# Optimization experiments

Measured on AMD Instinct MI355X. Metric: run time of the kernel, lower is better.

## Reference

```python
import jax, jax.numpy as jnp
import numpy as np

N_HEAD = 16

def setup_inputs() -> dict:
    key = jax.random.key(0)
    k1, k2, k3, k4, k5 = jax.random.split(key, 5)
    B, S, D = 2, 2048, 1024
    return {
        "hidden_states": jax.random.normal(k1, (B, S, D), jnp.float32),
        "w_attn": jax.random.normal(k2, (D, 3 * D), jnp.float32) * 0.02,
        "b_attn": jax.random.normal(k3, (3 * D,), jnp.float32) * 0.02,
        "w_proj": jax.random.normal(k4, (D, D), jnp.float32) * 0.02,
        "b_proj": jax.random.normal(k5, (D,), jnp.float32) * 0.02,
    }

def reference(hidden_states, w_attn, b_attn, w_proj, b_proj):
    B, S, D = hidden_states.shape
    H = N_HEAD
    Dh = D // H
    qkv = hidden_states @ w_attn + b_attn              # [B,S,3D]
    q, k, v = jnp.split(qkv, 3, axis=-1)
    def split_heads(x):
        return x.reshape(B, S, H, Dh).transpose(0, 2, 1, 3)  # [B,H,S,Dh]
    q, k, v = split_heads(q), split_heads(k), split_heads(v)
    # scale=True: divide by sqrt(head_dim) (v.size(-1))
    scores = jnp.einsum("bhqd,bhkd->bhqk", q, k) / jnp.sqrt(jnp.float32(Dh))
    attn = jax.nn.softmax(scores, axis=-1)             # [B,H,S,S]
    out = jnp.einsum("bhqk,bhkd->bhqd", attn, v)       # [B,H,S,Dh]
    out = out.transpose(0, 2, 1, 3).reshape(B, S, D)   # merge heads
    return out @ w_proj + b_proj
```

## Files before the change

### kernel.cpp

```cpp
#include <hip/hip_runtime.h>
#include <hip/hip_bf16.h>

typedef __attribute__((ext_vector_type(8))) short bf16x8;
typedef __attribute__((ext_vector_type(4))) float f32x4;
typedef __attribute__((ext_vector_type(16))) float f32x16;

#define LOG2E 1.4426950408889634f
#define SCALE_F (0.125f * LOG2E)

__device__ inline unsigned short f2bf(float f) {
  union { float f; unsigned u; } x; x.f = f;
  unsigned u = x.u;
  unsigned r = u + 0x7FFFu + ((u >> 16) & 1u);
  return (unsigned short)(r >> 16);
}

__device__ inline unsigned cvtpk(float lo, float hi) {
  unsigned r;
  asm("v_cvt_pk_bf16_f32 %0, %1, %2" : "=v"(r) : "v"(lo), "v"(hi));
  return r;
}

__device__ inline void gload16(const unsigned short* g, unsigned short* l) {
  __builtin_amdgcn_global_load_lds(
      (const __attribute__((address_space(1))) unsigned int*)g,
      (__attribute__((address_space(3))) unsigned int*)l, 16, 0, 0);
}

template <int J>
__device__ inline bf16x8 pack_pfrag(f32x16 p) {
  int X, Y, Z, W;
  asm("v_cvt_pk_bf16_f32 %0, %1, %2" : "=v"(X) : "v"(p[J + 0]), "v"(p[J + 1]));
  asm("v_cvt_pk_bf16_f32 %0, %1, %2" : "=v"(Y) : "v"(p[J + 2]), "v"(p[J + 3]));
  asm("v_cvt_pk_bf16_f32 %0, %1, %2" : "=v"(Z) : "v"(p[J + 4]), "v"(p[J + 5]));
  asm("v_cvt_pk_bf16_f32 %0, %1, %2" : "=v"(W) : "v"(p[J + 6]), "v"(p[J + 7]));
  asm("v_permlane32_swap_b32 %0, %1" : "+v"(X), "+v"(Z));
  asm("v_permlane32_swap_b32 %0, %1" : "+v"(Y), "+v"(W));
  union { int w[4]; bf16x8 v; } u;
  u.w[0] = X; u.w[1] = Y; u.w[2] = Z; u.w[3] = W;
  return u.v;
}

__device__ inline void transpose_tile(const float* __restrict__ W,
                                      unsigned short* __restrict__ WT, int K, int N,
                                      int n0, int k0, int t,
                                      unsigned short (*Tl)[72]) {
#pragma unroll
  for (int i = 0; i < 4; ++i) {
    int idx = t + i * 256;
    int r = idx >> 4, c4 = (idx & 15) << 2;
    float4 v = *reinterpret_cast<const float4*>(&W[(size_t)(k0 + r) * N + n0 + c4]);
    Tl[c4 + 0][r] = f2bf(v.x);
    Tl[c4 + 1][r] = f2bf(v.y);
    Tl[c4 + 2][r] = f2bf(v.z);
    Tl[c4 + 3][r] = f2bf(v.w);
  }
  __syncthreads();
#pragma unroll
  for (int i = 0; i < 2; ++i) {
    int idx = t + i * 256;
    int rr = idx >> 3, cc = (idx & 7) << 3;
    *reinterpret_cast<int4*>(&WT[(size_t)(n0 + rr) * K + k0 + cc]) =
        *reinterpret_cast<const int4*>(&Tl[rr][cc]);
  }
}

__global__ __launch_bounds__(256) void prep_fused(
    const float* __restrict__ hs, unsigned short* __restrict__ hs_b,
    const float* __restrict__ w_attn, unsigned short* __restrict__ wT,
    const float* __restrict__ w_proj, unsigned short* __restrict__ pT) {
  __shared__ unsigned short Tl[64][72];
  const int bid = blockIdx.x, t = threadIdx.x;
  if (bid < 768) {
    transpose_tile(w_attn, wT, 1024, 3072, (bid % 48) * 64, (bid / 48) * 64, t, Tl);
  } else if (bid < 1024) {
    int r = bid - 768;
    transpose_tile(w_proj, pT, 1024, 1024, (r % 16) * 64, (r / 16) * 64, t, Tl);
  } else {
    int cb = bid - 1024;
#pragma unroll
    for (int j = 0; j < 4; ++j) {
      int i = cb * 1024 + j * 256 + t;
      float4 v = reinterpret_cast<const float4*>(hs)[i];
      ushort4 o;
      o.x = f2bf(v.x); o.y = f2bf(v.y); o.z = f2bf(v.z); o.w = f2bf(v.w);
      reinterpret_cast<ushort4*>(hs_b)[i] = o;
    }
  }
}

__global__ __launch_bounds__(512, 2) void gemm_qkv_8p(
    const unsigned short* __restrict__ A, const unsigned short* __restrict__ Bt,
    const float* __restrict__ bias,
    unsigned short* __restrict__ qw, unsigned short* __restrict__ kw,
    unsigned short* __restrict__ vtg) {
  __shared__ unsigned short Abuf[2][16384];
  __shared__ unsigned short Bbuf[2][12288];
  const int t = threadIdx.x, lane = t & 63, wid = t >> 6;
  const int wm = wid >> 2, wn = wid & 3;
  const int orig = blockIdx.x;
  const int nid = (orig & 7) * 32 + (orig >> 3);
  const int mt = nid >> 4, nt = nid & 15;
  const int row0 = mt * 256, col0 = nt * 192;
  const int lr = lane & 15, kq = lane >> 4;
  const int srow_lo = lane >> 3;
  const int scg = (lane & 7) ^ srow_lo;
  const unsigned short* Ab = A + (size_t)row0 * 1024;
  const unsigned short* Bb = Bt + (size_t)col0 * 1024;
  f32x4 acc[8][3] = {};

#define SA8(bs, kt)                                                              \
  {                                                                              \
    const unsigned short* Ap = Ab + (kt) * 64;                                   \
    _Pragma("unroll") for (int i = 0; i < 4; ++i) {                              \
      int g = wid * 4 + i;                                                       \
      int rrel = g * 8 + srow_lo;                                                \
      gload16(&Ap[(size_t)rrel * 1024 + scg * 8], &Abuf[bs][g * 512]);           \
    }                                                                            \
  }
#define SB8(bs, kt)                                                              \
  {                                                                              \
    const unsigned short* Bp = Bb + (kt) * 64;                                   \
    _Pragma("unroll") for (int i = 0; i < 3; ++i) {                              \
      int g = wid * 3 + i;                                                       \
      int rrel = g * 8 + srow_lo;                                                \
      gload16(&Bp[(size_t)rrel * 1024 + scg * 8], &Bbuf[bs][g * 512]);           \
    }                                                                            \
  }
#define RDA(dst, mh)                                                             \
  _Pragma("unroll") for (int m = 0; m < 4; ++m)                                  \
  _Pragma("unroll") for (int ks = 0; ks < 2; ++ks) {                             \
    int row = wm * 128 + (mh) * 64 + m * 16 + lr;                                \
    dst[m][ks] = *reinterpret_cast<const bf16x8*>(                               \
        &Ac[row * 64 + (((ks * 4 + kq) ^ (row & 7)) << 3)]);                     \
  }
#define RDB2(dst)                                                                \
  _Pragma("unroll") for (int n = 0; n < 2; ++n)                                  \
  _Pragma("unroll") for (int ks = 0; ks < 2; ++ks) {                             \
    int row = wn * 48 + n * 16 + lr;                                             \
    dst[n][ks] = *reinterpret_cast<const bf16x8*>(                               \
        &Bc[row * 64 + (((ks * 4 + kq) ^ (row & 7)) << 3)]);                     \
  }
#define RDB1(dst)                                                                \
  _Pragma("unroll") for (int ks = 0; ks < 2; ++ks) {                             \
    int row = wn * 48 + 32 + lr;                                                 \
    dst[0][ks] = *reinterpret_cast<const bf16x8*>(                               \
        &Bc[row * 64 + (((ks * 4 + kq) ^ (row & 7)) << 3)]);                     \
  }
#define QMM2(mh, afv, bfv)                                                       \
  _Pragma("unroll") for (int m = 0; m < 4; ++m)                                  \
  _Pragma("unroll") for (int n = 0; n < 2; ++n)                                  \
  _Pragma("unroll") for (int ks = 0; ks < 2; ++ks)                               \
    acc[(mh) * 4 + m][n] = __builtin_amdgcn_mfma_f32_16x16x32_bf16(              \
        afv[m][ks], bfv[n][ks], acc[(mh) * 4 + m][n], 0, 0, 0);
#define QMM1(mh, afv, bfv)                                                       \
  _Pragma("unroll") for (int m = 0; m < 4; ++m)                                  \
  _Pragma("unroll") for (int ks = 0; ks < 2; ++ks)                               \
    acc[(mh) * 4 + m][2] = __builtin_amdgcn_mfma_f32_16x16x32_bf16(              \
        afv[m][ks], bfv[0][ks], acc[(mh) * 4 + m][2], 0, 0, 0);
#define BAR8 __builtin_amdgcn_s_barrier();

  SA8(0, 0) SB8(0, 0)
  asm volatile("s_waitcnt vmcnt(0)" ::: "memory");
  BAR8
  __builtin_amdgcn_sched_barrier(0);

  for (int kt = 0; kt < 16; ++kt) {
    const int buf = kt & 1;
    const unsigned short* Ac = Abuf[buf];
    const unsigned short* Bc = Bbuf[buf];
    bf16x8 af0[4][2], af1[4][2], bf0[2][2], bf1[1][2];
    RDA(af0, 0) RDB2(bf0)
    if (kt < 15) SA8(buf ^ 1, kt + 1)
    BAR8
    __builtin_amdgcn_s_setprio(1); QMM2(0, af0, bf0) __builtin_amdgcn_s_setprio(0);
    BAR8
    RDA(af1, 1)
    if (kt < 15) SB8(buf ^ 1, kt + 1)
    BAR8
    __builtin_amdgcn_s_setprio(1); QMM2(1, af1, bf0) __builtin_amdgcn_s_setprio(0);
    BAR8
    RDB1(bf1)
    BAR8
    __builtin_amdgcn_s_setprio(1); QMM1(0, af0, bf1) __builtin_amdgcn_s_setprio(0);
    BAR8
    if (kt < 15) { asm volatile("s_waitcnt vmcnt(0)" ::: "memory"); }
    BAR8
    __builtin_amdgcn_s_setprio(1); QMM1(1, af1, bf1) __builtin_amdgcn_s_setprio(0);
    BAR8
    __builtin_amdgcn_sched_barrier(0);
  }
#undef SA8
#undef SB8
#undef RDA
#undef RDB2
#undef RDB1
#undef QMM2
#undef QMM1
#undef BAR8

  const int rbase = (lane >> 4) * 4;
#pragma unroll
  for (int mm = 0; mm < 8; ++mm) {
#pragma unroll
    for (int nn = 0; nn < 3; ++nn) {
      int c = col0 + wn * 48 + nn * 16 + lr;
      int which = c >> 10;
      int d = c & 1023;
      int h = d >> 6, dh = d & 63;
      float bv = bias[c];
      int m0 = row0 + wm * 128 + mm * 16 + rbase;
      int b = m0 >> 11, s0 = m0 & 2047;
      if (which == 2) {
        int kt = s0 >> 6, key0 = s0 & 63;
        ushort4 pv;
        pv.x = f2bf(acc[mm][nn][0] + bv);
        pv.y = f2bf(acc[mm][nn][1] + bv);
        pv.z = f2bf(acc[mm][nn][2] + bv);
        pv.w = f2bf(acc[mm][nn][3] + bv);
        *reinterpret_cast<ushort4*>(
            &vtg[(((size_t)(b * 16 + h) * 32 + kt) * 64 + dh) * 64 + key0]) = pv;
      } else if (which == 1) {
#pragma unroll
        for (int r = 0; r < 4; ++r)
          kw[(((size_t)b * 16 + h) * 2048 + (s0 + r)) * 64 + dh] = f2bf(acc[mm][nn][r] + bv);
      } else {
#pragma unroll
        for (int r = 0; r < 4; ++r)
          qw[(((size_t)b * 16 + h) * 2048 + (s0 + r)) * 64 + dh] =
              f2bf((acc[mm][nn][r] + bv) * SCALE_F);
      }
    }
  }
}

__global__ __launch_bounds__(512, 4) void gemm_proj_8p(
    const unsigned short* __restrict__ A, const unsigned short* __restrict__ Bt,
    const float* __restrict__ bias, float* __restrict__ out) {
  __shared__ unsigned short Abuf[2][8192];
  __shared__ unsigned short Bbuf[2][8192];
  const int t = threadIdx.x, lane = t & 63, wid = t >> 6;
  const int wm = wid >> 2, wn = wid & 3;
  const int orig = blockIdx.x;
  const int nid = (orig & 7) * 32 + (orig >> 3);
  const int row0 = (nid >> 3) * 128, col0 = (nid & 7) * 128;
  const int lr = lane & 15, kq = lane >> 4;
  const int srow_lo = lane >> 3;
  const int scg = (lane & 7) ^ srow_lo;
  const unsigned short* Ab = A + (size_t)row0 * 1024;
  const unsigned short* Bb = Bt + (size_t)col0 * 1024;
  f32x4 acc[4][2] = {};

#define SP(bs, kt)                                                               \
  {                                                                              \
    const unsigned short* Ap = Ab + (kt) * 64;                                   \
    const unsigned short* Bp = Bb + (kt) * 64;                                   \
    _Pragma("unroll") for (int i = 0; i < 2; ++i) {                              \
      int g = wid * 2 + i;                                                       \
      int rrel = g * 8 + srow_lo;                                                \
      gload16(&Ap[(size_t)rrel * 1024 + scg * 8], &Abuf[bs][g * 512]);           \
      gload16(&Bp[(size_t)rrel * 1024 + scg * 8], &Bbuf[bs][g * 512]);           \
    }                                                                            \
  }
#define RPA(dst, mh)                                                             \
  _Pragma("unroll") for (int m = 0; m < 2; ++m)                                  \
  _Pragma("unroll") for (int ks = 0; ks < 2; ++ks) {                             \
    int row = wm * 64 + (mh) * 32 + m * 16 + lr;                                 \
    dst[m][ks] = *reinterpret_cast<const bf16x8*>(                               \
        &Ac[row * 64 + (((ks * 4 + kq) ^ (row & 7)) << 3)]);                     \
  }
#define RPB(dst)                                                                 \
  _Pragma("unroll") for (int n = 0; n < 2; ++n)                                  \
  _Pragma("unroll") for (int ks = 0; ks < 2; ++ks) {                             \
    int row = wn * 32 + n * 16 + lr;                                             \
    dst[n][ks] = *reinterpret_cast<const bf16x8*>(                               \
        &Bc[row * 64 + (((ks * 4 + kq) ^ (row & 7)) << 3)]);                     \
  }
#define PMM(mh, afv, bfv)                                                        \
  _Pragma("unroll") for (int m = 0; m < 2; ++m)                                  \
  _Pragma("unroll") for (int n = 0; n < 2; ++n)                                  \
  _Pragma("unroll") for (int ks = 0; ks < 2; ++ks)                               \
    acc[(mh) * 2 + m][n] = __builtin_amdgcn_mfma_f32_16x16x32_bf16(              \
        afv[m][ks], bfv[n][ks], acc[(mh) * 2 + m][n], 0, 0, 0);
#define BARP __builtin_amdgcn_s_barrier();

  SP(0, 0)
  asm volatile("s_waitcnt vmcnt(0)" ::: "memory");
  BARP
  __builtin_amdgcn_sched_barrier(0);

  for (int kt = 0; kt < 16; ++kt) {
    const int buf = kt & 1;
    const unsigned short* Ac = Abuf[buf];
    const unsigned short* Bc = Bbuf[buf];
    bf16x8 af0[2][2], af1[2][2], bfv[2][2];
    RPA(af0, 0) RPB(bfv)
    if (kt < 15) SP(buf ^ 1, kt + 1)
    BARP
    __builtin_amdgcn_s_setprio(1); PMM(0, af0, bfv) __builtin_amdgcn_s_setprio(0);
    BARP
    RPA(af1, 1)
    if (kt < 15) { asm volatile("s_waitcnt vmcnt(0)" ::: "memory"); }
    BARP
    __builtin_amdgcn_s_setprio(1); PMM(1, af1, bfv) __builtin_amdgcn_s_setprio(0);
    BARP
    __builtin_amdgcn_sched_barrier(0);
  }
#undef SP
#undef RPA
#undef RPB
#undef PMM
#undef BARP

  const int rbase = (lane >> 4) * 4;
#pragma unroll
  for (int mm = 0; mm < 4; ++mm) {
#pragma unroll
    for (int nn = 0; nn < 2; ++nn) {
      int c = col0 + wn * 32 + nn * 16 + lr;
      float bv = bias[c];
#pragma unroll
      for (int r = 0; r < 4; ++r) {
        int m = row0 + wm * 64 + mm * 16 + rbase + r;
        out[(size_t)m * 1024 + c] = acc[mm][nn][r] + bv;
      }
    }
  }
}

__global__ __launch_bounds__(512, 4) void attn_kernel(
    const unsigned short* __restrict__ qw, const unsigned short* __restrict__ kw,
    const unsigned short* __restrict__ vtg, unsigned short* __restrict__ ow) {
  __shared__ char smem[65536];
  unsigned short* KV = (unsigned short*)smem;
  unsigned short* Ol = (unsigned short*)smem;
  float* EX = (float*)(smem + 18432);
  const int t = threadIdx.x, lane = t & 63, wid = t >> 6;
  const int half = wid >> 2, wq = wid & 3;
  const int l31 = lane & 31, hi = lane >> 5;
  const int orig = blockIdx.x + 16 * blockIdx.y;
  const int nid = (orig & 7) * 64 + (orig >> 3);
  const int qt = nid & 15, bh = nid >> 4;
  const int b = bh >> 4, h = bh & 15;
  const unsigned short* Qg = qw + (size_t)bh * 2048 * 64;
  const unsigned short* Kg = kw + (size_t)bh * 2048 * 64;
  const unsigned short* Vg = vtg + (size_t)bh * 32 * 4096;
  const int q0 = qt * 128 + wq * 32;

  bf16x8 qf[4];
#pragma unroll
  for (int kc = 0; kc < 4; ++kc)
    qf[kc] = *reinterpret_cast<const bf16x8*>(&Qg[(q0 + l31) * 64 + kc * 16 + hi * 8]);

  f32x16 oA = {0,0,0,0,0,0,0,0,0,0,0,0,0,0,0,0};
  f32x16 oB = {0,0,0,0,0,0,0,0,0,0,0,0,0,0,0,0};
  float lrun = 0.f;

  const int srow_lo = lane >> 3;
  const int scg0 = (lane & 7) ^ srow_lo;
  const int rsw = (l31 & 7) ^ ((l31 >> 3) & 3);

#define STAGE(buf, kt)                                                              \
  {                                                                                 \
    const unsigned short* Kt = Kg + (size_t)(kt) * 4096;                            \
    const unsigned short* Vs = Vg + (size_t)(kt) * 4096;                            \
    unsigned short* Kl = KV + half * 16384 + (buf) * 8192;                          \
    unsigned short* Vl = Kl + 4096;                                                 \
    _Pragma("unroll") for (int i = 0; i < 2; ++i) {                                 \
      int chunk = wq * 2 + i;                                                       \
      int row = chunk * 8 + srow_lo;                                                \
      int sc = (scg0 ^ (chunk & 3)) * 8;                                            \
      gload16(&Kt[row * 64 + sc], &Kl[chunk * 512]);                                \
      gload16(&Vs[row * 64 + sc], &Vl[chunk * 512]);                                \
    }                                                                               \
  }

  const int kt0 = half * 16;
  STAGE(0, kt0)

  for (int it = 0; it < 16; ++it) {
    const int cur = it & 1;
    asm volatile("s_waitcnt vmcnt(0)" ::: "memory");
    __builtin_amdgcn_s_barrier();
    if (it + 1 < 16) STAGE(cur ^ 1, kt0 + it + 1)
    const unsigned short* Kl = KV + half * 16384 + cur * 8192;
    const unsigned short* Vl = Kl + 4096;

    f32x16 sA = {0,0,0,0,0,0,0,0,0,0,0,0,0,0,0,0};
    f32x16 sB = {0,0,0,0,0,0,0,0,0,0,0,0,0,0,0,0};
    __builtin_amdgcn_s_setprio(1);
#pragma unroll
    for (int kc = 0; kc < 4; ++kc) {
      bf16x8 k0f = *reinterpret_cast<const bf16x8*>(
          &Kl[l31 * 64 + (((kc * 2 + hi) ^ rsw) << 3)]);
      bf16x8 k1f = *reinterpret_cast<const bf16x8*>(
          &Kl[(32 + l31) * 64 + (((kc * 2 + hi) ^ rsw) << 3)]);
      sA = __builtin_amdgcn_mfma_f32_32x32x16_bf16(k0f, qf[kc], sA, 0, 0, 0);
      sB = __builtin_amdgcn_mfma_f32_32x32x16_bf16(k1f, qf[kc], sB, 0, 0, 0);
    }
    __builtin_amdgcn_s_setprio(0);

    float rsv[16];
#pragma unroll
    for (int j = 0; j < 16; ++j) {
      float pa = exp2f(sA[j]);
      float pb = exp2f(sB[j]);
      sA[j] = pa; sB[j] = pb;
      rsv[j] = pa + pb;
    }
#pragma unroll
    for (int s = 8; s >= 1; s >>= 1)
#pragma unroll
      for (int j = 0; j < s; ++j) rsv[j] += rsv[j + s];
    lrun += rsv[0] + __shfl_xor(rsv[0], 32);

    bf16x8 pf0 = pack_pfrag<0>(sA);
    bf16x8 pf1 = pack_pfrag<8>(sA);
    bf16x8 pf2 = pack_pfrag<0>(sB);
    bf16x8 pf3 = pack_pfrag<8>(sB);

    __builtin_amdgcn_s_setprio(1);
#pragma unroll
    for (int c = 0; c < 4; ++c) {
      bf16x8 pf = (c == 0) ? pf0 : (c == 1) ? pf1 : (c == 2) ? pf2 : pf3;
      int g = c * 2 + hi;
      bf16x8 v0f = *reinterpret_cast<const bf16x8*>(
          &Vl[l31 * 64 + ((g ^ rsw) << 3)]);
      bf16x8 v1f = *reinterpret_cast<const bf16x8*>(
          &Vl[(32 + l31) * 64 + ((g ^ rsw) << 3)]);
      oA = __builtin_amdgcn_mfma_f32_32x32x16_bf16(v0f, pf, oA, 0, 0, 0);
      oB = __builtin_amdgcn_mfma_f32_32x32x16_bf16(v1f, pf, oB, 0, 0, 0);
    }
    __builtin_amdgcn_s_setprio(0);
  }
#undef STAGE

  __syncthreads();
  if (half == 1) {
    float* e = EX + ((size_t)(wq * 64 + lane)) * 34;
#pragma unroll
    for (int j = 0; j < 16; ++j) { e[j] = oA[j]; e[16 + j] = oB[j]; }
    e[32] = lrun;
  }
  __syncthreads();
  if (half == 0) {
    const float* e = EX + ((size_t)(wq * 64 + lane)) * 34;
    float linv = 1.0f / (lrun + e[32]);
    unsigned short* orow_l = Ol + (wq * 32 + l31) * 72;
#pragma unroll
    for (int g = 0; g < 4; ++g) {
      float a0 = (oA[4 * g + 0] + e[4 * g + 0]) * linv;
      float a1v = (oA[4 * g + 1] + e[4 * g + 1]) * linv;
      float a2v = (oA[4 * g + 2] + e[4 * g + 2]) * linv;
      float a3v = (oA[4 * g + 3] + e[4 * g + 3]) * linv;
      uint2 w0; w0.x = cvtpk(a0, a1v); w0.y = cvtpk(a2v, a3v);
      *reinterpret_cast<uint2*>(&orow_l[8 * g + 4 * hi]) = w0;
      float b0 = (oB[4 * g + 0] + e[16 + 4 * g + 0]) * linv;
      float b1v = (oB[4 * g + 1] + e[16 + 4 * g + 1]) * linv;
      float b2v = (oB[4 * g + 2] + e[16 + 4 * g + 2]) * linv;
      float b3v = (oB[4 * g + 3] + e[16 + 4 * g + 3]) * linv;
      uint2 w1; w1.x = cvtpk(b0, b1v); w1.y = cvtpk(b2v, b3v);
      *reinterpret_cast<uint2*>(&orow_l[32 + 8 * g + 4 * hi]) = w1;
    }
  }
  __syncthreads();
#pragma unroll
  for (int i = 0; i < 2; ++i) {
    int idx = t + i * 512;
    int q = idx >> 3, ch = idx & 7;
    int4 v = *reinterpret_cast<const int4*>(&Ol[q * 72 + ch * 8]);
    *reinterpret_cast<int4*>(
        &ow[(((size_t)b * 2048 + qt * 128 + q) * 16 + h) * 64 + ch * 8]) = v;
  }
}

extern "C" void kernel_launch(void* const* d_in, const int* in_sizes, int n_in,
                              void* d_out, int out_size, void* d_ws, size_t ws_size,
                              hipStream_t stream) {
  const float* hs = (const float*)d_in[0];
  const float* w_attn = (const float*)d_in[1];
  const float* b_attn = (const float*)d_in[2];
  const float* w_proj = (const float*)d_in[3];
  const float* b_proj = (const float*)d_in[4];
  float* out = (float*)d_out;

  const size_t HEAD = (size_t)2 * 16 * 2048 * 64;
  unsigned short* qw = (unsigned short*)d_ws;
  unsigned short* kw = qw + HEAD;
  unsigned short* vtg = kw + HEAD;
  unsigned short* hs_b = vtg + HEAD;
  unsigned short* ow = hs_b;
  unsigned short* wT = hs_b + HEAD;
  unsigned short* pT = wT + (size_t)3072 * 1024;

  prep_fused<<<dim3(2048), 256, 0, stream>>>(hs, hs_b, w_attn, wT, w_proj, pT);

  gemm_qkv_8p<<<dim3(256), 512, 0, stream>>>(hs_b, wT, b_attn, qw, kw, vtg);
  attn_kernel<<<dim3(16, 32), 512, 0, stream>>>(qw, kw, vtg, ow);
  gemm_proj_8p<<<dim3(256), 512, 0, stream>>>(ow, pT, b_proj, out);
}
```

Before: 115.3 us.

## Load V fragments directly from global memory and drop one GEMM barrier

The attention kernel stops staging V tiles through LDS. Each wave now reads its V fragments straight from global memory into registers, with half issued before the QK MFMAs and half after softmax, and the K prefetch is moved later in the iteration. This halves the LDS footprint and removes the LDS write/read traffic for V, at the cost of exposed global-load latency and more VGPRs. In both projection GEMMs the vmcnt wait is moved after the last MFMA group, and in the QKV GEMM one barrier is removed, to overlap the final compute with outstanding loads.

Result: slower. 145.5 us (+26.2%).

```diff
diff --git a/kernel.cpp b/kernel.cpp
--- a/kernel.cpp
+++ b/kernel.cpp
@@ -184,9 +184,8 @@
     BAR8
     __builtin_amdgcn_s_setprio(1); QMM1(0, af0, bf1) __builtin_amdgcn_s_setprio(0);
     BAR8
+    __builtin_amdgcn_s_setprio(1); QMM1(1, af1, bf1) __builtin_amdgcn_s_setprio(0);
     if (kt < 15) { asm volatile("s_waitcnt vmcnt(0)" ::: "memory"); }
-    BAR8
-    __builtin_amdgcn_s_setprio(1); QMM1(1, af1, bf1) __builtin_amdgcn_s_setprio(0);
     BAR8
     __builtin_amdgcn_sched_barrier(0);
   }
@@ -300,9 +299,9 @@
     __builtin_amdgcn_s_setprio(1); PMM(0, af0, bfv) __builtin_amdgcn_s_setprio(0);
     BARP
     RPA(af1, 1)
-    if (kt < 15) { asm volatile("s_waitcnt vmcnt(0)" ::: "memory"); }
     BARP
     __builtin_amdgcn_s_setprio(1); PMM(1, af1, bfv) __builtin_amdgcn_s_setprio(0);
+    if (kt < 15) { asm volatile("s_waitcnt vmcnt(0)" ::: "memory"); }
     BARP
     __builtin_amdgcn_sched_barrier(0);
   }
@@ -331,8 +330,8 @@
 __global__ __launch_bounds__(512, 4) void attn_kernel(
     const unsigned short* __restrict__ qw, const unsigned short* __restrict__ kw,
     const unsigned short* __restrict__ vtg, unsigned short* __restrict__ ow) {
-  __shared__ char smem[65536];
-  unsigned short* KV = (unsigned short*)smem;
+  __shared__ char smem[53248];
+  unsigned short* KB = (unsigned short*)smem;
   unsigned short* Ol = (unsigned short*)smem;
   float* EX = (float*)(smem + 18432);
   const int t = threadIdx.x, lane = t & 63, wid = t >> 6;
@@ -360,31 +359,31 @@
   const int scg0 = (lane & 7) ^ srow_lo;
   const int rsw = (l31 & 7) ^ ((l31 >> 3) & 3);
 
-#define STAGE(buf, kt)                                                              \
+#define KSTAGE(buf, kt)                                                             \
   {                                                                                 \
     const unsigned short* Kt = Kg + (size_t)(kt) * 4096;                            \
-    const unsigned short* Vs = Vg + (size_t)(kt) * 4096;                            \
-    unsigned short* Kl = KV + half * 16384 + (buf) * 8192;                          \
-    unsigned short* Vl = Kl + 4096;                                                 \
+    unsigned short* Kl = KB + half * 8192 + (buf) * 4096;                           \
     _Pragma("unroll") for (int i = 0; i < 2; ++i) {                                 \
       int chunk = wq * 2 + i;                                                       \
       int row = chunk * 8 + srow_lo;                                                \
       int sc = (scg0 ^ (chunk & 3)) * 8;                                            \
       gload16(&Kt[row * 64 + sc], &Kl[chunk * 512]);                                \
-      gload16(&Vs[row * 64 + sc], &Vl[chunk * 512]);                                \
     }                                                                               \
   }
 
   const int kt0 = half * 16;
-  STAGE(0, kt0)
+  KSTAGE(0, kt0)
 
   for (int it = 0; it < 16; ++it) {
     const int cur = it & 1;
     asm volatile("s_waitcnt vmcnt(0)" ::: "memory");
     __builtin_amdgcn_s_barrier();
-    if (it + 1 < 16) STAGE(cur ^ 1, kt0 + it + 1)
-    const unsigned short* Kl = KV + half * 16384 + cur * 8192;
-    const unsigned short* Vl = Kl + 4096;
+    const unsigned short* Vt = Vg + (size_t)(kt0 + it) * 4096;
+    bf16x8 vf0 = *reinterpret_cast<const bf16x8*>(&Vt[l31 * 64 + hi * 8]);
+    bf16x8 vf1 = *reinterpret_cast<const bf16x8*>(&Vt[(32 + l31) * 64 + hi * 8]);
+    bf16x8 vf2 = *reinterpret_cast<const bf16x8*>(&Vt[l31 * 64 + (2 + hi) * 8]);
+    bf16x8 vf3 = *reinterpret_cast<const bf16x8*>(&Vt[(32 + l31) * 64 + (2 + hi) * 8]);
+    const unsigned short* Kl = KB + half * 8192 + cur * 4096;
 
     f32x16 sA = {0,0,0,0,0,0,0,0,0,0,0,0,0,0,0,0};
     f32x16 sB = {0,0,0,0,0,0,0,0,0,0,0,0,0,0,0,0};
@@ -419,21 +418,24 @@
     bf16x8 pf2 = pack_pfrag<0>(sB);
     bf16x8 pf3 = pack_pfrag<8>(sB);
 
+    bf16x8 vf4 = *reinterpret_cast<const bf16x8*>(&Vt[l31 * 64 + (4 + hi) * 8]);
+    bf16x8 vf5 = *reinterpret_cast<const bf16x8*>(&Vt[(32 + l31) * 64 + (4 + hi) * 8]);
+    bf16x8 vf6 = *reinterpret_cast<const bf16x8*>(&Vt[l31 * 64 + (6 + hi) * 8]);
+    bf16x8 vf7 = *reinterpret_cast<const bf16x8*>(&Vt[(32 + l31) * 64 + (6 + hi) * 8]);
+    if (it + 1 < 16) KSTAGE(cur ^ 1, kt0 + it + 1)
+
     __builtin_amdgcn_s_setprio(1);
-#pragma unroll
-    for (int c = 0; c < 4; ++c) {
-      bf16x8 pf = (c == 0) ? pf0 : (c == 1) ? pf1 : (c == 2) ? pf2 : pf3;
-      int g = c * 2 + hi;
-      bf16x8 v0f = *reinterpret_cast<const bf16x8*>(
-          &Vl[l31 * 64 + ((g ^ rsw) << 3)]);
-      bf16x8 v1f = *reinterpret_cast<const bf16x8*>(
-          &Vl[(32 + l31) * 64 + ((g ^ rsw) << 3)]);
-      oA = __builtin_amdgcn_mfma_f32_32x32x16_bf16(v0f, pf, oA, 0, 0, 0);
-      oB = __builtin_amdgcn_mfma_f32_32x32x16_bf16(v1f, pf, oB, 0, 0, 0);
-    }
+    oA = __builtin_amdgcn_mfma_f32_32x32x16_bf16(vf0, pf0, oA, 0, 0, 0);
+    oB = __builtin_amdgcn_mfma_f32_32x32x16_bf16(vf1, pf0, oB, 0, 0, 0);
+    oA = __builtin_amdgcn_mfma_f32_32x32x16_bf16(vf2, pf1, oA, 0, 0, 0);
+    oB = __builtin_amdgcn_mfma_f32_32x32x16_bf16(vf3, pf1, oB, 0, 0, 0);
+    oA = __builtin_amdgcn_mfma_f32_32x32x16_bf16(vf4, pf2, oA, 0, 0, 0);
+    oB = __builtin_amdgcn_mfma_f32_32x32x16_bf16(vf5, pf2, oB, 0, 0, 0);
+    oA = __builtin_amdgcn_mfma_f32_32x32x16_bf16(vf6, pf3, oA, 0, 0, 0);
+    oB = __builtin_amdgcn_mfma_f32_32x32x16_bf16(vf7, pf3, oB, 0, 0, 0);
     __builtin_amdgcn_s_setprio(0);
   }
-#undef STAGE
+#undef KSTAGE
 
   __syncthreads();
   if (half == 1) {
```
